# Kernel optimization log

Measured on AMD Instinct MI355X. Metric: run time of the kernel, lower is better.

## Reference

```python
import jax, jax.numpy as jnp
import numpy as np

D_MODEL = 1024
N_HEADS = 16
HEAD_DIM = D_MODEL // N_HEADS
B, S = 4, 2048
NEG = -1000000000.0


def setup_inputs() -> dict:
    key = jax.random.key(0)
    ks = jax.random.split(key, 13)
    sc = 1.0 / np.sqrt(D_MODEL)
    return {
        "query": jax.random.normal(ks[0], (B, S, D_MODEL), jnp.float32),
        "key": jax.random.normal(ks[1], (B, S, D_MODEL), jnp.float32),
        "value": jax.random.normal(ks[2], (B, S, D_MODEL), jnp.float32),
        "mask": jax.random.randint(ks[3], (B, 1, 1, S), 0, 2, jnp.int32),
        "Wq": jax.random.normal(ks[4], (D_MODEL, D_MODEL), jnp.float32) * sc,
        "bq": jax.random.normal(ks[5], (D_MODEL,), jnp.float32) * sc,
        "Wk": jax.random.normal(ks[6], (D_MODEL, D_MODEL), jnp.float32) * sc,
        "bk": jax.random.normal(ks[7], (D_MODEL,), jnp.float32) * sc,
        "Wv": jax.random.normal(ks[8], (D_MODEL, D_MODEL), jnp.float32) * sc,
        "bv": jax.random.normal(ks[9], (D_MODEL,), jnp.float32) * sc,
        "Wo": jax.random.normal(ks[10], (D_MODEL, D_MODEL), jnp.float32) * sc,
        "bo": jax.random.normal(ks[11], (D_MODEL,), jnp.float32) * sc,
    }


def _split_heads(x):
    b, s, _ = x.shape
    return x.reshape(b, s, N_HEADS, HEAD_DIM).transpose(0, 2, 1, 3)  # (B,H,S,Dh)


def reference(query, key, value, mask, Wq, bq, Wk, bk, Wv, bv, Wo, bo):
    # torch Linear: y = x @ W.T + b
    Q = _split_heads(query @ Wq.T + bq)
    K = _split_heads(key @ Wk.T + bk)
    V = _split_heads(value @ Wv.T + bv)
    scores = jnp.einsum("bhqd,bhkd->bhqk", Q, K) / np.sqrt(HEAD_DIM)
    scores = jnp.where(mask == 0, NEG, scores)
    probs = jax.nn.softmax(scores, axis=-1)
    ctx = jnp.einsum("bhqk,bhkd->bhqd", probs, V)
    ctx = ctx.transpose(0, 2, 1, 3).reshape(query.shape[0], query.shape[1], D_MODEL)
    return ctx @ Wo.T + bo
```

## Files before the change

### kernel.cpp

```cpp
#include <hip/hip_runtime.h>


typedef __bf16 bf16x8 __attribute__((ext_vector_type(8)));
typedef __bf16 bf16x4 __attribute__((ext_vector_type(4)));
typedef float  f32x4  __attribute__((ext_vector_type(4)));

#define LOG2E 1.44269504088896340736f
#define SCALE_Q (0.125f * LOG2E)
#define MBIAS_L2 (-1.44269504e9f)

__device__ inline unsigned short f2bf(float f) {
  unsigned int u = __float_as_uint(f);
  u = u + 0x7FFF + ((u >> 16) & 1);
  return (unsigned short)(u >> 16);
}
__device__ inline void gload16(const void* g, void* l) {
  __builtin_amdgcn_global_load_lds(
      (const __attribute__((address_space(1))) void*)g,
      (__attribute__((address_space(3))) void*)l, 16, 0, 0);
}
__device__ inline bf16x8 cvt8(const float* p) {
  float4 a = *(const float4*)p, b = *(const float4*)(p + 4);
  bf16x8 v;
  v[0] = (__bf16)a.x; v[1] = (__bf16)a.y; v[2] = (__bf16)a.z; v[3] = (__bf16)a.w;
  v[4] = (__bf16)b.x; v[5] = (__bf16)b.y; v[6] = (__bf16)b.z; v[7] = (__bf16)b.w;
  return v;
}

struct CvtJob { const float* s; unsigned short* d; int n8; };
struct CvtJobs { CvtJob j[7]; };
__global__ void cvt_all(CvtJobs J) {
  CvtJob jb = J.j[blockIdx.y];
  int i = blockIdx.x * 256 + threadIdx.x;
  if (i < jb.n8) *(bf16x8*)(jb.d + (size_t)i * 8) = cvt8(jb.s + (size_t)i * 8);
}

struct ProjJob { const unsigned short* A; const unsigned short* W;
                 const float* bias; unsigned short* out; float scale; };
struct ProjJobs { ProjJob j[3]; };

__global__ __launch_bounds__(256, 2) void gemm_qkv(ProjJobs J) {
  __shared__ __align__(16) unsigned short Al[128 * 32];
  __shared__ __align__(16) unsigned short Wl[128 * 32];
  const int z = blockIdx.z;
  const ProjJob jb = J.j[z];
  const int tid = threadIdx.x, lane = tid & 63, w = tid >> 6;
  const int lid = lane & 15, lg = lane >> 4;
  const int c0 = blockIdx.x * 128, t0 = blockIdx.y * 128;
  const int wm = (w & 1) * 64, wn = (w >> 1) * 64;
  const unsigned short* Ml = (z == 2) ? Al : Wl;
  const unsigned short* Nl = (z == 2) ? Wl : Al;

  f32x4 acc[4][4];
#pragma unroll
  for (int i = 0; i < 4; i++)
#pragma unroll
    for (int j = 0; j < 4; j++) acc[i][j] = (f32x4){0.f, 0.f, 0.f, 0.f};

  for (int kt = 0; kt < 1024; kt += 32) {
    __syncthreads();
#pragma unroll
    for (int i = 0; i < 2; i++) {
      int c = i * 256 + tid, r = c >> 2, ko = (c & 3) * 8;
      gload16(jb.A + (size_t)(t0 + r) * 1024 + kt + ko, &Al[c * 8]);
      gload16(jb.W + (size_t)(c0 + r) * 1024 + kt + ko, &Wl[c * 8]);
    }
    __syncthreads();
    bf16x8 mf[4], nf[4];
#pragma unroll
    for (int mi = 0; mi < 4; mi++)
      mf[mi] = *(const bf16x8*)(&Ml[(wm + mi * 16 + lid) * 32 + lg * 8]);
#pragma unroll
    for (int ni = 0; ni < 4; ni++)
      nf[ni] = *(const bf16x8*)(&Nl[(wn + ni * 16 + lid) * 32 + lg * 8]);
#pragma unroll
    for (int mi = 0; mi < 4; mi++)
#pragma unroll
      for (int ni = 0; ni < 4; ni++)
        acc[mi][ni] = __builtin_amdgcn_mfma_f32_16x16x32_bf16(mf[mi], nf[ni],
                                                              acc[mi][ni], 0, 0, 0);
  }

  if (z < 2) {
    const float scale = jb.scale;
#pragma unroll
    for (int mi = 0; mi < 4; mi++) {
      int colb = c0 + wm + mi * 16 + lg * 4;
      float4 b4 = *(const float4*)(&jb.bias[colb]);
#pragma unroll
      for (int ni = 0; ni < 4; ni++) {
        int token = t0 + wn + ni * 16 + lid;
        ushort4 st;
        st.x = f2bf((acc[mi][ni][0] + b4.x) * scale);
        st.y = f2bf((acc[mi][ni][1] + b4.y) * scale);
        st.z = f2bf((acc[mi][ni][2] + b4.z) * scale);
        st.w = f2bf((acc[mi][ni][3] + b4.w) * scale);
        *(ushort4*)(&jb.out[(size_t)token * 1024 + colb]) = st;
      }
    }
  } else {
    const int b = t0 >> 11;
#pragma unroll
    for (int ni = 0; ni < 4; ni++) {
      int col = c0 + wn + ni * 16 + lid;
      int h = col >> 6, d = col & 63;
      float bv = jb.bias[col];
#pragma unroll
      for (int mi = 0; mi < 4; mi++) {
        int s = (t0 & 2047) + wm + mi * 16 + lg * 4;
        ushort4 st;
        st.x = f2bf(acc[mi][ni][0] + bv);
        st.y = f2bf(acc[mi][ni][1] + bv);
        st.z = f2bf(acc[mi][ni][2] + bv);
        st.w = f2bf(acc[mi][ni][3] + bv);
        *(ushort4*)(&jb.out[(size_t)((b * 16 + h) * 64 + d) * 2048 + s]) = st;
      }
    }
  }
}

__global__ __launch_bounds__(256, 2) void gemm_o(
    const unsigned short* __restrict__ A, const unsigned short* __restrict__ W,
    const float* __restrict__ bias, float* __restrict__ C) {
  __shared__ __align__(16) unsigned short Al[128 * 32];
  __shared__ __align__(16) unsigned short Wl[128 * 32];
  const int tid = threadIdx.x, lane = tid & 63, w = tid >> 6;
  const int lid = lane & 15, lg = lane >> 4;
  const int c0 = blockIdx.x * 128, t0 = blockIdx.y * 128;
  const int wc = (w & 1) * 64, wt = (w >> 1) * 64;
  f32x4 acc[4][4];
#pragma unroll
  for (int i = 0; i < 4; i++)
#pragma unroll
    for (int j = 0; j < 4; j++) acc[i][j] = (f32x4){0.f, 0.f, 0.f, 0.f};

  for (int kt = 0; kt < 1024; kt += 32) {
    __syncthreads();
#pragma unroll
    for (int i = 0; i < 2; i++) {
      int c = i * 256 + tid, r = c >> 2, ko = (c & 3) * 8;
      gload16(A + (size_t)(t0 + r) * 1024 + kt + ko, &Al[c * 8]);
      gload16(W + (size_t)(c0 + r) * 1024 + kt + ko, &Wl[c * 8]);
    }
    __syncthreads();
    bf16x8 aw[4], bt[4];
#pragma unroll
    for (int mi = 0; mi < 4; mi++)
      aw[mi] = *(const bf16x8*)(&Wl[(wc + mi * 16 + lid) * 32 + lg * 8]);
#pragma unroll
    for (int ni = 0; ni < 4; ni++)
      bt[ni] = *(const bf16x8*)(&Al[(wt + ni * 16 + lid) * 32 + lg * 8]);
#pragma unroll
    for (int mi = 0; mi < 4; mi++)
#pragma unroll
      for (int ni = 0; ni < 4; ni++)
        acc[mi][ni] = __builtin_amdgcn_mfma_f32_16x16x32_bf16(aw[mi], bt[ni],
                                                              acc[mi][ni], 0, 0, 0);
  }
#pragma unroll
  for (int mi = 0; mi < 4; mi++) {
    int colb = c0 + wc + mi * 16 + lg * 4;
    float4 b4 = *(const float4*)(&bias[colb]);
#pragma unroll
    for (int ni = 0; ni < 4; ni++) {
      int token = t0 + wt + ni * 16 + lid;
      float4 st;
      st.x = acc[mi][ni][0] + b4.x;
      st.y = acc[mi][ni][1] + b4.y;
      st.z = acc[mi][ni][2] + b4.z;
      st.w = acc[mi][ni][3] + b4.w;
      *(float4*)(&C[(size_t)token * 1024 + colb]) = st;
    }
  }
}

__global__ __launch_bounds__(256, 2) void attn(
    const unsigned short* __restrict__ Qp,
    const unsigned short* __restrict__ Kp,
    const unsigned short* __restrict__ Vt,
    const int* __restrict__ maskp,
    unsigned short* __restrict__ ctx) {
  __shared__ __align__(16) unsigned short Klds[2][64 * 64];
  __shared__ __align__(16) unsigned short Vlds[2][64 * 64];
  __shared__ __align__(16) float mball[2048];

  const int tid = threadIdx.x, lane = tid & 63, w = tid >> 6;
  const int lid = lane & 15, lg = lane >> 4;
  const int q0 = blockIdx.x * 128, bh = blockIdx.y;
  const int b = bh >> 4, h = bh & 15;
  const int wq = w * 32;
  const int x7 = lid & 7;

  const unsigned short* Kg = Kp + (size_t)(b * 2048) * 1024 + h * 64;
  const unsigned short* Vg = Vt + (size_t)bh * 64 * 2048;
  const int* mg = maskp + b * 2048;

#pragma unroll
  for (int i = 0; i < 8; i++) {
    int idx = i * 256 + tid;
    mball[idx] = (mg[idx] == 0) ? MBIAS_L2 : 0.0f;
  }

  bf16x8 qf[2][2];
#pragma unroll
  for (int nt = 0; nt < 2; nt++)
#pragma unroll
    for (int ks = 0; ks < 2; ks++) {
      int qrow = b * 2048 + q0 + wq + nt * 16 + lid;
      qf[nt][ks] = *(const bf16x8*)(Qp + (size_t)qrow * 1024 + h * 64 + ks * 32 + lg * 8);
    }

  f32x4 Ot[4][2];
#pragma unroll
  for (int dt = 0; dt < 4; dt++)
#pragma unroll
    for (int qt = 0; qt < 2; qt++) Ot[dt][qt] = (f32x4){0.f, 0.f, 0.f, 0.f};
  f32x4 acc_l[2] = {(f32x4){0.f, 0.f, 0.f, 0.f}, (f32x4){0.f, 0.f, 0.f, 0.f}};
  bf16x8 ones8;
#pragma unroll
  for (int i = 0; i < 8; i++) ones8[i] = (__bf16)1.0f;

  auto stage_kv = [&](unsigned short* Kl, unsigned short* Vl, int k0) {
#pragma unroll
    for (int i = 0; i < 2; i++) {
      int c = i * 256 + tid, r = c >> 3, gsw = (c & 7) ^ (r & 7);
      gload16(Kg + (size_t)(k0 + r) * 1024 + gsw * 8, Kl + c * 8);
    }
#pragma unroll
    for (int i = 0; i < 2; i++) {
      int c = i * 256 + tid, d = c >> 3, gsw = (c & 7) ^ (d & 7);
      gload16(Vg + (size_t)d * 2048 + k0 + gsw * 8, Vl + c * 8);
    }
  };

  auto compute_tile = [&](const unsigned short* Kl, const unsigned short* Vl,
                          int kt) {
    const float* mb = mball + kt * 64;
    f32x4 accS[4][2];
#pragma unroll
    for (int mt = 0; mt < 4; mt++) {
      const f32x4 mb4 = *(const f32x4*)(&mb[mt * 16 + lg * 4]);
      accS[mt][0] = mb4;
      accS[mt][1] = mb4;
    }
    __builtin_amdgcn_s_setprio(1);
#pragma unroll
    for (int ks = 0; ks < 2; ks++) {
      int koff = ((ks * 4 + lg) ^ x7) * 8;
#pragma unroll
      for (int mt = 0; mt < 4; mt++) {
        bf16x8 a = *(const bf16x8*)(&Kl[(mt * 16 + lid) * 64 + koff]);
        accS[mt][0] = __builtin_amdgcn_mfma_f32_16x16x32_bf16(a, qf[0][ks], accS[mt][0], 0, 0, 0);
        accS[mt][1] = __builtin_amdgcn_mfma_f32_16x16x32_bf16(a, qf[1][ks], accS[mt][1], 0, 0, 0);
      }
    }
    __builtin_amdgcn_s_setprio(0);

    bf16x8 pb[2][2];
#pragma unroll
    for (int nt = 0; nt < 2; nt++) {
#pragma unroll
      for (int mt = 0; mt < 4; mt++) {
        int half = (mt & 1) * 4;
#pragma unroll
        for (int r = 0; r < 4; r++) {
          float p = __builtin_amdgcn_exp2f(accS[mt][nt][r]);
          pb[mt >> 1][nt][half + r] = (__bf16)p;
        }
      }
    }

    __builtin_amdgcn_s_setprio(1);
#pragma unroll
    for (int c = 0; c < 2; c++)
#pragma unroll
      for (int qt = 0; qt < 2; qt++)
        acc_l[qt] = __builtin_amdgcn_mfma_f32_16x16x32_bf16(ones8, pb[c][qt], acc_l[qt], 0, 0, 0);

#pragma unroll
    for (int c = 0; c < 2; c++) {
      int glo = ((4 * c + (lg >> 1)) ^ x7) * 8 + (lg & 1) * 4;
      int ghi = ((4 * c + 2 + (lg >> 1)) ^ x7) * 8 + (lg & 1) * 4;
#pragma unroll
      for (int dt = 0; dt < 4; dt++) {
        const unsigned short* vrow = &Vl[(dt * 16 + lid) * 64];
        bf16x4 lo = *(const bf16x4*)(&vrow[glo]);
        bf16x4 hi = *(const bf16x4*)(&vrow[ghi]);
        bf16x8 av = __builtin_shufflevector(lo, hi, 0, 1, 2, 3, 4, 5, 6, 7);
#pragma unroll
        for (int qt = 0; qt < 2; qt++)
          Ot[dt][qt] = __builtin_amdgcn_mfma_f32_16x16x32_bf16(av, pb[c][qt], Ot[dt][qt], 0, 0, 0);
      }
    }
    __builtin_amdgcn_s_setprio(0);
  };

  stage_kv(Klds[0], Vlds[0], 0);
  __syncthreads();

  for (int kt = 0; kt < 32; kt += 2) {
    stage_kv(Klds[1], Vlds[1], (kt + 1) * 64);
    compute_tile(Klds[0], Vlds[0], kt);
    __syncthreads();
    if (kt + 2 < 32) stage_kv(Klds[0], Vlds[0], (kt + 2) * 64);
    compute_tile(Klds[1], Vlds[1], kt + 1);
    __syncthreads();
  }

#pragma unroll
  for (int qt = 0; qt < 2; qt++) {
    float inv = 1.0f / acc_l[qt][0];
    int qrow = b * 2048 + q0 + wq + qt * 16 + lid;
#pragma unroll
    for (int dt = 0; dt < 4; dt++) {
      ushort4 st;
      st.x = f2bf(Ot[dt][qt][0] * inv);
      st.y = f2bf(Ot[dt][qt][1] * inv);
      st.z = f2bf(Ot[dt][qt][2] * inv);
      st.w = f2bf(Ot[dt][qt][3] * inv);
      *(ushort4*)(&ctx[(size_t)qrow * 1024 + h * 64 + dt * 16 + lg * 4]) = st;
    }
  }
}

extern "C" void kernel_launch(void* const* d_in, const int* in_sizes, int n_in,
                              void* d_out, int out_size, void* d_ws, size_t ws_size,
                              hipStream_t stream) {
  const float* q  = (const float*)d_in[0];
  const float* k  = (const float*)d_in[1];
  const float* v  = (const float*)d_in[2];
  const int*   mk = (const int*)d_in[3];
  const float* Wq = (const float*)d_in[4];
  const float* bq = (const float*)d_in[5];
  const float* Wk = (const float*)d_in[6];
  const float* bk = (const float*)d_in[7];
  const float* Wv = (const float*)d_in[8];
  const float* bv = (const float*)d_in[9];
  const float* Wo = (const float*)d_in[10];
  const float* bo = (const float*)d_in[11];

  const size_t NTOK = (size_t)8192 * 1024;
  const size_t NW = (size_t)1024 * 1024;

  unsigned short* qb  = (unsigned short*)d_ws;
  unsigned short* kb  = qb + NTOK;
  unsigned short* vb  = kb + NTOK;
  unsigned short* Qp  = vb + NTOK;
  unsigned short* Kp  = Qp + NTOK;
  unsigned short* Vt  = Kp + NTOK;
  unsigned short* Wqb = Vt + NTOK;
  unsigned short* Wkb = Wqb + NW;
  unsigned short* Wvb = Wkb + NW;
  unsigned short* Wob = Wvb + NW;
  unsigned short* ctx = qb;

  CvtJobs J;
  J.j[0] = {q, qb, (int)(NTOK / 8)};
  J.j[1] = {k, kb, (int)(NTOK / 8)};
  J.j[2] = {v, vb, (int)(NTOK / 8)};
  J.j[3] = {Wq, Wqb, (int)(NW / 8)};
  J.j[4] = {Wk, Wkb, (int)(NW / 8)};
  J.j[5] = {Wv, Wvb, (int)(NW / 8)};
  J.j[6] = {Wo, Wob, (int)(NW / 8)};
  cvt_all<<<dim3(4096, 7), 256, 0, stream>>>(J);

  ProjJobs P;
  P.j[0] = {qb, Wqb, bq, Qp, SCALE_Q};
  P.j[1] = {kb, Wkb, bk, Kp, 1.0f};
  P.j[2] = {vb, Wvb, bv, Vt, 1.0f};
  gemm_qkv<<<dim3(8, 64, 3), 256, 0, stream>>>(P);

  attn<<<dim3(16, 64), 256, 0, stream>>>(Qp, Kp, Vt, mk, ctx);
  gemm_o<<<dim3(8, 64), 256, 0, stream>>>(ctx, Wob, bo, (float*)d_out);
}
```

Before: 354.1 us.

## Software-pipeline attention QK/softmax/PV across tiles, remap blocks per XCD, precompute mask bias

Restructures the attention loop so that the QK^T of tile k overlaps with the PV of tile k-1. K and V are staged separately, and P is double-buffered in registers. The per-block LDS mask-bias array is removed in favour of a float bias vector precomputed once in the conversion kernel and read from global memory. The change also remaps block indices so that heads are grouped per XCD for L2 locality, and raises launch bounds to 4 blocks per CU. Together these aim to hide exp/MFMA latency, cut LDS usage and redundant mask work, and improve cache reuse, but they raise register pressure and could spill under the tighter occupancy bound.

```diff
diff --git a/kernel.cpp b/kernel.cpp
--- a/kernel.cpp
+++ b/kernel.cpp
@@ -8,6 +8,7 @@
 #define LOG2E 1.44269504088896340736f
 #define SCALE_Q (0.125f * LOG2E)
 #define MBIAS_L2 (-1.44269504e9f)
+#define MFMA16(a, b, c) __builtin_amdgcn_mfma_f32_16x16x32_bf16(a, b, c, 0, 0, 0)
 
 __device__ inline unsigned short f2bf(float f) {
   unsigned int u = __float_as_uint(f);
@@ -28,10 +29,22 @@
 }
 
 struct CvtJob { const float* s; unsigned short* d; int n8; };
-struct CvtJobs { CvtJob j[7]; };
+struct CvtJobs { CvtJob j[8]; };
 __global__ void cvt_all(CvtJobs J) {
   CvtJob jb = J.j[blockIdx.y];
   int i = blockIdx.x * 256 + threadIdx.x;
+  if (blockIdx.y == 7) {
+    if (i < jb.n8) {
+      int4 m = ((const int4*)jb.s)[i];
+      float4 o;
+      o.x = m.x ? 0.f : MBIAS_L2;
+      o.y = m.y ? 0.f : MBIAS_L2;
+      o.z = m.z ? 0.f : MBIAS_L2;
+      o.w = m.w ? 0.f : MBIAS_L2;
+      ((float4*)jb.d)[i] = o;
+    }
+    return;
+  }
   if (i < jb.n8) *(bf16x8*)(jb.d + (size_t)i * 8) = cvt8(jb.s + (size_t)i * 8);
 }
 
@@ -77,8 +90,7 @@
     for (int mi = 0; mi < 4; mi++)
 #pragma unroll
       for (int ni = 0; ni < 4; ni++)
-        acc[mi][ni] = __builtin_amdgcn_mfma_f32_16x16x32_bf16(mf[mi], nf[ni],
-                                                              acc[mi][ni], 0, 0, 0);
+        acc[mi][ni] = MFMA16(mf[mi], nf[ni], acc[mi][ni]);
   }
 
   if (z < 2) {
@@ -154,8 +166,7 @@
     for (int mi = 0; mi < 4; mi++)
 #pragma unroll
       for (int ni = 0; ni < 4; ni++)
-        acc[mi][ni] = __builtin_amdgcn_mfma_f32_16x16x32_bf16(aw[mi], bt[ni],
-                                                              acc[mi][ni], 0, 0, 0);
+        acc[mi][ni] = MFMA16(aw[mi], bt[ni], acc[mi][ni]);
   }
 #pragma unroll
   for (int mi = 0; mi < 4; mi++) {
@@ -174,32 +185,28 @@
   }
 }
 
-__global__ __launch_bounds__(256, 2) void attn(
+__global__ __launch_bounds__(256, 4) void attn(
     const unsigned short* __restrict__ Qp,
     const unsigned short* __restrict__ Kp,
     const unsigned short* __restrict__ Vt,
-    const int* __restrict__ maskp,
+    const float* __restrict__ mbias,
     unsigned short* __restrict__ ctx) {
   __shared__ __align__(16) unsigned short Klds[2][64 * 64];
   __shared__ __align__(16) unsigned short Vlds[2][64 * 64];
-  __shared__ __align__(16) float mball[2048];
 
   const int tid = threadIdx.x, lane = tid & 63, w = tid >> 6;
   const int lid = lane & 15, lg = lane >> 4;
-  const int q0 = blockIdx.x * 128, bh = blockIdx.y;
+  const int wg = blockIdx.x + (int)(gridDim.x) * blockIdx.y;
+  const int xcd = wg & 7, idx = wg >> 3;
+  const int bh = (xcd << 3) | (idx >> 4);
+  const int q0 = (idx & 15) * 128;
   const int b = bh >> 4, h = bh & 15;
   const int wq = w * 32;
   const int x7 = lid & 7;
 
   const unsigned short* Kg = Kp + (size_t)(b * 2048) * 1024 + h * 64;
   const unsigned short* Vg = Vt + (size_t)bh * 64 * 2048;
-  const int* mg = maskp + b * 2048;
-
-#pragma unroll
-  for (int i = 0; i < 8; i++) {
-    int idx = i * 256 + tid;
-    mball[idx] = (mg[idx] == 0) ? MBIAS_L2 : 0.0f;
-  }
+  const float* mg = mbias + b * 2048;
 
   bf16x8 qf[2][2];
 #pragma unroll
@@ -220,12 +227,14 @@
 #pragma unroll
   for (int i = 0; i < 8; i++) ones8[i] = (__bf16)1.0f;
 
-  auto stage_kv = [&](unsigned short* Kl, unsigned short* Vl, int k0) {
+  auto stage_K = [&](unsigned short* Kl, int k0) {
 #pragma unroll
     for (int i = 0; i < 2; i++) {
       int c = i * 256 + tid, r = c >> 3, gsw = (c & 7) ^ (r & 7);
       gload16(Kg + (size_t)(k0 + r) * 1024 + gsw * 8, Kl + c * 8);
     }
+  };
+  auto stage_V = [&](unsigned short* Vl, int k0) {
 #pragma unroll
     for (int i = 0; i < 2; i++) {
       int c = i * 256 + tid, d = c >> 3, gsw = (c & 7) ^ (d & 7);
@@ -233,13 +242,11 @@
     }
   };
 
-  auto compute_tile = [&](const unsigned short* Kl, const unsigned short* Vl,
-                          int kt) {
-    const float* mb = mball + kt * 64;
-    f32x4 accS[4][2];
+  auto qk = [&](int kt, const unsigned short* Kl, f32x4 (&accS)[4][2]) {
+    const float* mrow = mg + kt * 64;
 #pragma unroll
     for (int mt = 0; mt < 4; mt++) {
-      const f32x4 mb4 = *(const f32x4*)(&mb[mt * 16 + lg * 4]);
+      f32x4 mb4 = *(const f32x4*)(&mrow[mt * 16 + lg * 4]);
       accS[mt][0] = mb4;
       accS[mt][1] = mb4;
     }
@@ -250,33 +257,20 @@
 #pragma unroll
       for (int mt = 0; mt < 4; mt++) {
         bf16x8 a = *(const bf16x8*)(&Kl[(mt * 16 + lid) * 64 + koff]);
-        accS[mt][0] = __builtin_amdgcn_mfma_f32_16x16x32_bf16(a, qf[0][ks], accS[mt][0], 0, 0, 0);
-        accS[mt][1] = __builtin_amdgcn_mfma_f32_16x16x32_bf16(a, qf[1][ks], accS[mt][1], 0, 0, 0);
+        accS[mt][0] = MFMA16(a, qf[0][ks], accS[mt][0]);
+        accS[mt][1] = MFMA16(a, qf[1][ks], accS[mt][1]);
       }
     }
     __builtin_amdgcn_s_setprio(0);
-
-    bf16x8 pb[2][2];
-#pragma unroll
-    for (int nt = 0; nt < 2; nt++) {
-#pragma unroll
-      for (int mt = 0; mt < 4; mt++) {
-        int half = (mt & 1) * 4;
-#pragma unroll
-        for (int r = 0; r < 4; r++) {
-          float p = __builtin_amdgcn_exp2f(accS[mt][nt][r]);
-          pb[mt >> 1][nt][half + r] = (__bf16)p;
-        }
-      }
-    }
-
+  };
+
+  auto pv = [&](bf16x8 (&pb)[2][2], const unsigned short* Vl) {
     __builtin_amdgcn_s_setprio(1);
 #pragma unroll
     for (int c = 0; c < 2; c++)
 #pragma unroll
       for (int qt = 0; qt < 2; qt++)
-        acc_l[qt] = __builtin_amdgcn_mfma_f32_16x16x32_bf16(ones8, pb[c][qt], acc_l[qt], 0, 0, 0);
-
+        acc_l[qt] = MFMA16(ones8, pb[c][qt], acc_l[qt]);
 #pragma unroll
     for (int c = 0; c < 2; c++) {
       int glo = ((4 * c + (lg >> 1)) ^ x7) * 8 + (lg & 1) * 4;
@@ -289,23 +283,48 @@
         bf16x8 av = __builtin_shufflevector(lo, hi, 0, 1, 2, 3, 4, 5, 6, 7);
 #pragma unroll
         for (int qt = 0; qt < 2; qt++)
-          Ot[dt][qt] = __builtin_amdgcn_mfma_f32_16x16x32_bf16(av, pb[c][qt], Ot[dt][qt], 0, 0, 0);
+          Ot[dt][qt] = MFMA16(av, pb[c][qt], Ot[dt][qt]);
       }
     }
     __builtin_amdgcn_s_setprio(0);
   };
 
-  stage_kv(Klds[0], Vlds[0], 0);
+  auto sm = [&](f32x4 (&accS)[4][2], bf16x8 (&pbCur)[2][2]) {
+#pragma unroll
+    for (int nt = 0; nt < 2; nt++)
+#pragma unroll
+      for (int mt = 0; mt < 4; mt++) {
+        int half = (mt & 1) * 4;
+#pragma unroll
+        for (int r = 0; r < 4; r++) {
+          float p = __builtin_amdgcn_exp2f(accS[mt][nt][r]);
+          pbCur[mt >> 1][nt][half + r] = (__bf16)p;
+        }
+      }
+  };
+
+  bf16x8 pbA[2][2], pbB[2][2];
+
+  auto body = [&](int kt, int kb, auto& pbPrev, auto& pbCur, int first, int last) {
+    if (!last) stage_K(&Klds[kb ^ 1][0], (kt + 1) * 64);
+    stage_V(&Vlds[kb][0], kt * 64);
+    f32x4 accS[4][2];
+    qk(kt, &Klds[kb][0], accS);
+    if (!first) pv(pbPrev, &Vlds[kb ^ 1][0]);
+    sm(accS, pbCur);
+    __syncthreads();
+  };
+
+  stage_K(&Klds[0][0], 0);
   __syncthreads();
 
-  for (int kt = 0; kt < 32; kt += 2) {
-    stage_kv(Klds[1], Vlds[1], (kt + 1) * 64);
-    compute_tile(Klds[0], Vlds[0], kt);
-    __syncthreads();
-    if (kt + 2 < 32) stage_kv(Klds[0], Vlds[0], (kt + 2) * 64);
-    compute_tile(Klds[1], Vlds[1], kt + 1);
-    __syncthreads();
-  }
+  body(0, 0, pbB, pbA, 1, 0);
+  for (int kt = 1; kt < 31; kt += 2) {
+    body(kt, 1, pbA, pbB, 0, 0);
+    body(kt + 1, 0, pbB, pbA, 0, 0);
+  }
+  body(31, 1, pbA, pbB, 0, 1);
+  pv(pbB, &Vlds[1][0]);
 
 #pragma unroll
   for (int qt = 0; qt < 2; qt++) {
@@ -352,6 +371,7 @@
   unsigned short* Wkb = Wqb + NW;
   unsigned short* Wvb = Wkb + NW;
   unsigned short* Wob = Wvb + NW;
+  float*          mbg = (float*)(Wob + NW);
   unsigned short* ctx = qb;
 
   CvtJobs J;
@@ -362,7 +382,8 @@
   J.j[4] = {Wk, Wkb, (int)(NW / 8)};
   J.j[5] = {Wv, Wvb, (int)(NW / 8)};
   J.j[6] = {Wo, Wob, (int)(NW / 8)};
-  cvt_all<<<dim3(4096, 7), 256, 0, stream>>>(J);
+  J.j[7] = {(const float*)mk, (unsigned short*)mbg, 2048};
+  cvt_all<<<dim3(4096, 8), 256, 0, stream>>>(J);
 
   ProjJobs P;
   P.j[0] = {qb, Wqb, bq, Qp, SCALE_Q};
@@ -370,6 +391,6 @@
   P.j[2] = {vb, Wvb, bv, Vt, 1.0f};
   gemm_qkv<<<dim3(8, 64, 3), 256, 0, stream>>>(P);
 
-  attn<<<dim3(16, 64), 256, 0, stream>>>(Qp, Kp, Vt, mk, ctx);
+  attn<<<dim3(16, 64), 256, 0, stream>>>(Qp, Kp, Vt, mbg, ctx);
   gemm_o<<<dim3(8, 64), 256, 0, stream>>>(ctx, Wob, bo, (float*)d_out);
 }
```

Result: slower. 501.8 us (+41.7%).
